# Optimization experiments

Hardware: AMD Instinct MI355X
Metric: run time of the kernel (lower is better)

## Reference

```python
import jax, jax.numpy as jnp
import numpy as np

H_DIM = 256
N_HEADS = 8
HALF = H_DIM // 2

def _lin(x, W, b):
    # torch nn.Linear: y = x @ W.T + b
    y = x @ W.T
    return y + b if b is not None else y

def setup_inputs() -> dict:
    key = jax.random.key(0)
    ks = jax.random.split(key, 16)
    s = 0.02
    d = {
        'x': jax.random.normal(ks[0], (16, H_DIM, 32, 32), jnp.float32),
        'q1_w': jax.random.normal(ks[1], (HALF, HALF), jnp.float32) * s,
        'q1_b': jnp.zeros((HALF,), jnp.float32),
        'q2_w': jax.random.normal(ks[2], (HALF, HALF), jnp.float32) * s,
        'q2_b': jnp.zeros((HALF,), jnp.float32),
        'k1_w': jax.random.normal(ks[3], (HALF, HALF), jnp.float32) * s,
        'k1_b': jnp.zeros((HALF,), jnp.float32),
        'k2_w': jax.random.normal(ks[4], (HALF, HALF), jnp.float32) * s,
        'k2_b': jnp.zeros((HALF,), jnp.float32),
        'v1_w': jax.random.normal(ks[5], (HALF, HALF), jnp.float32) * s,
        'v1_b': jnp.zeros((HALF,), jnp.float32),
        'v2_w': jax.random.normal(ks[6], (HALF, HALF), jnp.float32) * s,
        'v2_b': jnp.zeros((HALF,), jnp.float32),
        'proj1_w': jax.random.normal(ks[7], (HALF, HALF), jnp.float32) * s,
        'proj1_b': jnp.zeros((HALF,), jnp.float32),
        'proj2_w': jax.random.normal(ks[8], (HALF, HALF), jnp.float32) * s,
        'proj2_b': jnp.zeros((HALF,), jnp.float32),
        'logit_scale': jnp.log(10.0 * jnp.ones((N_HEADS, 1, 1), jnp.float32)),
        'mlp_w1': jax.random.normal(ks[9], (128, 2), jnp.float32) * s,
        'mlp_b1': jnp.zeros((128,), jnp.float32),
        'mlp_w2': jax.random.normal(ks[10], (N_HEADS, 128), jnp.float32) * s,
    }
    return d

def _rel_pos_index(h, w):
    # static (numpy) relative position index, shape [N, N]
    ch, cw = np.meshgrid(np.arange(h), np.arange(w), indexing='ij')
    coords = np.stack([ch.reshape(-1), cw.reshape(-1)])  # [2, N]
    rel = coords[:, :, None] - coords[:, None, :]         # [2, N, N]
    rel = rel.transpose(1, 2, 0)
    rel[:, :, 0] += h - 1
    rel[:, :, 1] += w - 1
    return rel[:, :, 0] * (2 * w - 1) + rel[:, :, 1]

def _forward(x, q1_w, q1_b, q2_w, q2_b, k1_w, k1_b, k2_w, k2_b,
             v1_w, v1_b, v2_w, v2_b, proj1_w, proj1_b, proj2_w, proj2_b,
             logit_scale, mlp_w1, mlp_b1, mlp_w2):
    b, c, h, w = x.shape
    N = h * w
    nh = N_HEADS
    hd = c // nh
    x3 = jnp.transpose(x, (0, 2, 3, 1)).reshape(b, N, c)
    x0, x1 = x3[..., :c // 2], x3[..., c // 2:]

    def qkv(W0, b0, W1, b1):
        t = jnp.concatenate([x0 + _lin(x0, W0, b0), x1 + _lin(x1, W1, b1)], axis=-1)
        return t.reshape(b, N, nh, hd).transpose(0, 2, 1, 3)  # [b, nh, N, hd]

    q = qkv(q1_w, q1_b, q2_w, q2_b)
    k = qkv(k1_w, k1_b, k2_w, k2_b)
    v = qkv(v1_w, v1_b, v2_w, v2_b)

    eps = 1e-12
    qn = q / jnp.maximum(jnp.linalg.norm(q, axis=-1, keepdims=True), eps)
    kn = k / jnp.maximum(jnp.linalg.norm(k, axis=-1, keepdims=True), eps)
    attn = jnp.einsum('bhnd,bhmd->bhnm', qn, kn)  # cosine similarity
    scale = jnp.exp(jnp.minimum(logit_scale, jnp.log(1.0 / 0.01)))  # [nh,1,1]
    attn = attn * scale[None]

    # continuous relative-position bias (CPB) table via small MLP
    rch = jnp.arange(-(h - 1), h, dtype=jnp.float32) / (h - 1 + 1e-8)
    rcw = jnp.arange(-(w - 1), w, dtype=jnp.float32) / (w - 1 + 1e-8)
    gh, gw = jnp.meshgrid(rch, rcw, indexing='ij')
    tab = jnp.stack([gh, gw], axis=-1) * 3.2               # [2h-1, 2w-1, 2]
    tab = jnp.sign(tab) * (1.0 - jnp.exp(-jnp.abs(tab)))
    tab = jax.nn.relu(_lin(tab, mlp_w1, mlp_b1))
    tab = _lin(tab, mlp_w2, None).reshape(-1, nh)          # [(2h-1)(2w-1), nh]

    idx = jnp.asarray(_rel_pos_index(h, w))                # [N, N]
    bias = tab[idx.reshape(-1)].reshape(N, N, nh).transpose(2, 0, 1)
    bias = 16.0 * jax.nn.sigmoid(bias)
    attn = attn + bias[None]

    attn = jax.nn.softmax(attn, axis=-1)
    out = jnp.einsum('bhnm,bhmd->bhnd', attn, v).transpose(0, 2, 1, 3).reshape(b, N, c)
    o0, o1 = out[..., :c // 2], out[..., c // 2:]
    out = jnp.concatenate([_lin(o0, proj1_w, proj1_b), _lin(o1, proj2_w, proj2_b)], axis=-1)
    return out.reshape(b, h, w, c).transpose(0, 3, 1, 2)

def reference(x, q1_w, q1_b, q2_w, q2_b, k1_w, k1_b, k2_w, k2_b,
              v1_w, v1_b, v2_w, v2_b, proj1_w, proj1_b, proj2_w, proj2_b,
              logit_scale, mlp_w1, mlp_b1, mlp_w2):
    return _forward(x, q1_w, q1_b, q2_w, q2_b, k1_w, k1_b, k2_w, k2_b,
                    v1_w, v1_b, v2_w, v2_b, proj1_w, proj1_b, proj2_w, proj2_b,
                    logit_scale, mlp_w1, mlp_b1, mlp_w2)
```

## Files before the change

### kernel.cpp

```cpp
#include <hip/hip_runtime.h>
#include <cmath>


typedef _Float16 half_t;
typedef __attribute__((ext_vector_type(4))) _Float16 half4;
typedef __attribute__((ext_vector_type(8))) _Float16 half8;
typedef __attribute__((ext_vector_type(4))) float float4v;

static __device__ __forceinline__ float4v mfma16(half8 a, half8 b, float4v c) {
  return __builtin_amdgcn_mfma_f32_16x16x32_f16(a, b, c, 0, 0, 0);
}

struct PtrArr8 { const float* p[8]; };

__global__ __launch_bounds__(256) void prep_w(PtrArr8 wsrc, PtrArr8 bsrc,
                                              half_t* __restrict__ wf,
                                              float* __restrict__ bws) {
  int y = blockIdx.y;
  const float* src = nullptr;
  const float* bs = nullptr;
#pragma unroll
  for (int i = 0; i < 8; i++)
    if (i == y) { src = wsrc.p[i]; bs = bsrc.p[i]; }
  int i0 = (blockIdx.x * 256 + threadIdx.x) * 4;
  float4 w = *(const float4*)(src + i0);
  int j = i0 >> 7, k = i0 & 127;
  float id0 = 0.f, id1 = 0.f, id2 = 0.f, id3 = 0.f;
  if (y < 6) {
    if (j == k)     id0 = 1.0f;
    if (j == k + 1) id1 = 1.0f;
    if (j == k + 2) id2 = 1.0f;
    if (j == k + 3) id3 = 1.0f;
  }
  half4 h;
  h[0] = (half_t)(w.x + id0);
  h[1] = (half_t)(w.y + id1);
  h[2] = (half_t)(w.z + id2);
  h[3] = (half_t)(w.w + id3);
  *(half4*)(wf + y * 16384 + i0) = h;
  if (blockIdx.x == 0 && threadIdx.x < 128)
    bws[y * 128 + threadIdx.x] = bs[threadIdx.x];
}

__global__ __launch_bounds__(256) void bias_mlp(const float* __restrict__ w1,
                                                const float* __restrict__ b1,
                                                const float* __restrict__ w2,
                                                float* __restrict__ tabh) {
  __shared__ float sw1[256];
  __shared__ float sb1[128];
  __shared__ float sw2[1024];
  int t = threadIdx.x;
  sw1[t] = w1[t];
  if (t < 128) sb1[t] = b1[t];
  for (int i = t; i < 1024; i += 256) sw2[i] = w2[i];
  __syncthreads();
  int p = blockIdx.x * 256 + t;
  if (p >= 3969) return;
  int ph = p / 63, pw = p % 63;
  float t0 = (float)(ph - 31) * (3.2f / 31.0f);
  float t1 = (float)(pw - 31) * (3.2f / 31.0f);
  t0 = copysignf(1.0f - __expf(-fabsf(t0)), t0);
  t1 = copysignf(1.0f - __expf(-fabsf(t1)), t1);
  float acc[8];
#pragma unroll
  for (int hh = 0; hh < 8; hh++) acc[hh] = 0.0f;
  for (int j = 0; j < 128; j++) {
    float hj = fmaxf(0.0f, t0 * sw1[2 * j] + t1 * sw1[2 * j + 1] + sb1[j]);
#pragma unroll
    for (int hh = 0; hh < 8; hh++) acc[hh] += hj * sw2[hh * 128 + j];
  }
#pragma unroll
  for (int hh = 0; hh < 8; hh++)
    tabh[hh * 3969 + p] = 16.0f / (1.0f + __expf(-acc[hh]));
}

__global__ __launch_bounds__(256) void qkv_mfma(
    const float* __restrict__ x, const half_t* __restrict__ wf,
    const float* __restrict__ lscale, const float* __restrict__ bws,
    half_t* __restrict__ qf, half_t* __restrict__ kf,
    half_t* __restrict__ vf) {
  __shared__ half_t yt[128 * 68];
  int t = threadIdx.x;
  int lane = t & 63, wv = t >> 6, l = lane & 15, quad = lane >> 4;
  int m0 = blockIdx.x * 64;
  int b = m0 >> 10, n0 = m0 & 1023;

  half8 afr[8];
  {
    const float* xb = x + (size_t)b * 256 * 1024 + n0 + wv * 16 + l;
#pragma unroll
    for (int hf = 0; hf < 2; hf++)
#pragma unroll
      for (int ks = 0; ks < 4; ks++) {
        int kbase = hf * 128 + ks * 32 + quad * 8;
        half8 a;
#pragma unroll
        for (int j = 0; j < 8; j++)
          a[j] = (half_t)xb[(size_t)(kbase + j) * 1024];
        afr[hf * 4 + ks] = a;
      }
  }

#pragma unroll
  for (int combo = 0; combo < 6; combo++) {
    int op = combo >> 1, hf = combo & 1;
    const half_t* wl = wf + combo * 16384 + l * 128 + quad * 8;
    float4v acc[8];
#pragma unroll
    for (int ng = 0; ng < 8; ng++) {
      float4v c = {0.f, 0.f, 0.f, 0.f};
#pragma unroll
      for (int ks = 0; ks < 4; ks++) {
        half8 bfrag = *(const half8*)(wl + ng * 2048 + ks * 32);
        c = mfma16(afr[hf * 4 + ks], bfrag, c);
      }
      acc[ng] = c;
    }
#pragma unroll
    for (int ng = 0; ng < 8; ng++) {
      float bb = bws[combo * 128 + ng * 16 + l];
#pragma unroll
      for (int r2 = 0; r2 < 4; r2++) acc[ng][r2] += bb;
    }
    if (op < 2) {
#pragma unroll
      for (int hg = 0; hg < 4; hg++) {
        float sc = 1.0f;
        if (op == 0)
          sc = __expf(fminf(lscale[hf * 4 + hg], 4.6051702f));
#pragma unroll
        for (int r2 = 0; r2 < 4; r2++) {
          float ss = acc[2 * hg][r2] * acc[2 * hg][r2] +
                     acc[2 * hg + 1][r2] * acc[2 * hg + 1][r2];
          ss += __shfl_xor(ss, 1, 64);
          ss += __shfl_xor(ss, 2, 64);
          ss += __shfl_xor(ss, 4, 64);
          ss += __shfl_xor(ss, 8, 64);
          float rn = sc / fmaxf(sqrtf(ss), 1e-12f);
          acc[2 * hg][r2] *= rn;
          acc[2 * hg + 1][r2] *= rn;
        }
      }
      half_t* dst = (op == 0) ? qf : kf;
#pragma unroll
      for (int ng = 0; ng < 8; ng++) {
        int head = hf * 4 + (ng >> 1);
        int d = (ng & 1) * 16 + l;
        size_t base =
            (((size_t)b * 8 + head) * 1024 + n0 + wv * 16 + quad * 4) * 32 + d;
#pragma unroll
        for (int r2 = 0; r2 < 4; r2++)
          dst[base + (size_t)r2 * 32] = (half_t)acc[ng][r2];
      }
    } else {
#pragma unroll
      for (int ng = 0; ng < 8; ng++) {
        int col = ng * 16 + l;
        half4 hv;
#pragma unroll
        for (int r2 = 0; r2 < 4; r2++) hv[r2] = (half_t)acc[ng][r2];
        *(half4*)(yt + col * 68 + wv * 16 + quad * 4) = hv;
      }
      __syncthreads();
#pragma unroll
      for (int i = 0; i < 16; i++) {
        int idx = t + 256 * i;
        int col = idx >> 5, rp = idx & 31;
        unsigned int val = *(const unsigned int*)(yt + col * 68 + rp * 2);
        int head = hf * 4 + (col >> 5);
        int d = col & 31;
        *(unsigned int*)((char*)vf +
                         (((((size_t)b * 8 + head) * 32 + d) * 1024) + n0 +
                          rp * 2) * 2) = val;
      }
      __syncthreads();
    }
  }
}

__global__ __launch_bounds__(256) void attn_mfma(
    const half_t* __restrict__ qf, const half_t* __restrict__ kf,
    const half_t* __restrict__ vf, const float* __restrict__ tabh,
    half_t* __restrict__ ao) {
  __shared__ half_t kb[64 * 40];
  __shared__ half_t vt[32 * 72];
  __shared__ half_t pa[4 * 16 * 72];
  __shared__ float sbias[192];

  int t = threadIdx.x;
  int lane = t & 63, wv = t >> 6, l = lane & 15, quad = lane >> 4;
  int qt = blockIdx.x, h = blockIdx.y, b = blockIdx.z;
  int n0 = qt * 64;
  size_t bh = (size_t)b * 8 + h;

  half8 qfr =
      *(const half8*)(qf + (bh * 1024 + n0 + wv * 16 + l) * 32 + quad * 8);

  int qrow_loc = wv * 16 + l;
  int iwq = qrow_loc & 31;
  int ihl = qrow_loc >> 5;

  float run_m = -1e30f, run_l = 0.0f;
  float4v o0 = {0.f, 0.f, 0.f, 0.f}, o1 = {0.f, 0.f, 0.f, 0.f};
  half_t* paw = pa + wv * 16 * 72;

  for (int kt = 0; kt < 16; kt++) {
    __syncthreads();
    {
      int key = t >> 2, dg = t & 3;
      half8 kd =
          *(const half8*)(kf + (bh * 1024 + kt * 64 + key) * 32 + dg * 8);
      *(half8*)(kb + key * 40 + dg * 8) = kd;
      int vd = t >> 3, kg = t & 7;
      half8 vdv =
          *(const half8*)(vf + (bh * 32 + vd) * 1024 + kt * 64 + kg * 8);
      *(half8*)(vt + vd * 72 + kg * 8) = vdv;
      if (t < 189) {
        int r3 = (t >= 126) ? 2 : ((t >= 63) ? 1 : 0);
        int pw = t - r3 * 63;
        int dih = 2 * (qt - kt) + 30 + r3;
        sbias[t] = tabh[h * 3969 + dih * 63 + pw];
      }
    }
    __syncthreads();

    float4v s[4];
#pragma unroll
    for (int nt = 0; nt < 4; nt++) {
      half8 kfr = *(const half8*)(kb + (nt * 16 + l) * 40 + quad * 8);
      float4v z = {0.f, 0.f, 0.f, 0.f};
      s[nt] = mfma16(kfr, qfr, z);
    }
    float lmax = -1e30f;
#pragma unroll
    for (int nt = 0; nt < 4; nt++) {
      int dih_off = ihl - (nt >> 1) + 1;
      int base = dih_off * 63 + iwq + 31 - ((nt & 1) * 16 + 4 * quad);
#pragma unroll
      for (int r2 = 0; r2 < 4; r2++) {
        float v = s[nt][r2] + sbias[base - r2];
        s[nt][r2] = v;
        lmax = fmaxf(lmax, v);
      }
    }
    lmax = fmaxf(lmax, __shfl_xor(lmax, 16, 64));
    lmax = fmaxf(lmax, __shfl_xor(lmax, 32, 64));
    float new_m = fmaxf(run_m, lmax);
    float alpha = __expf(run_m - new_m);
    float lsum = 0.0f;
#pragma unroll
    for (int nt = 0; nt < 4; nt++) {
      half4 ph;
#pragma unroll
      for (int r2 = 0; r2 < 4; r2++) {
        float p = __expf(s[nt][r2] - new_m);
        lsum += p;
        ph[r2] = (half_t)p;
      }
      *(half4*)(paw + l * 72 + nt * 16 + quad * 4) = ph;
    }
    lsum += __shfl_xor(lsum, 16, 64);
    lsum += __shfl_xor(lsum, 32, 64);
    run_l = run_l * alpha + lsum;
    run_m = new_m;
#pragma unroll
    for (int r2 = 0; r2 < 4; r2++) {
      float ar = __shfl(alpha, 20 * quad + r2, 64);
      o0[r2] *= ar;
      o1[r2] *= ar;
    }
#pragma unroll
    for (int ks = 0; ks < 2; ks++) {
      half8 pfr = *(const half8*)(paw + l * 72 + ks * 32 + quad * 8);
      half8 v0f = *(const half8*)(vt + l * 72 + ks * 32 + quad * 8);
      half8 v1f = *(const half8*)(vt + (16 + l) * 72 + ks * 32 + quad * 8);
      o0 = mfma16(pfr, v0f, o0);
      o1 = mfma16(pfr, v1f, o1);
    }
  }

  float rli = 1.0f / run_l;
#pragma unroll
  for (int r2 = 0; r2 < 4; r2++) {
    float linv = __shfl(rli, 20 * quad + r2, 64);
    size_t rowaddr =
        ((size_t)b * 1024 + n0 + wv * 16 + quad * 4 + r2) * 256 + h * 32;
    ao[rowaddr + l] = (half_t)(o0[r2] * linv);
    ao[rowaddr + 16 + l] = (half_t)(o1[r2] * linv);
  }
}

__global__ __launch_bounds__(256) void proj_mfma(
    const half_t* __restrict__ ao, const half_t* __restrict__ wp,
    const float* __restrict__ bws, float* __restrict__ out) {
  __shared__ float yt[128 * 68];
  int t = threadIdx.x;
  int lane = t & 63, wv = t >> 6, l = lane & 15, quad = lane >> 4;
  int m0 = blockIdx.x * 64;
  int b = m0 >> 10, n0 = m0 & 1023;

#pragma unroll
  for (int hf = 0; hf < 2; hf++) {
    half8 afr[4];
    const half_t* ab =
        ao + ((size_t)m0 + wv * 16 + l) * 256 + hf * 128 + quad * 8;
#pragma unroll
    for (int ks = 0; ks < 4; ks++) afr[ks] = *(const half8*)(ab + ks * 32);
    const half_t* wl = wp + hf * 16384 + l * 128 + quad * 8;
#pragma unroll
    for (int ng = 0; ng < 8; ng++) {
      float4v c = {0.f, 0.f, 0.f, 0.f};
#pragma unroll
      for (int ks = 0; ks < 4; ks++)
        c = mfma16(afr[ks], *(const half8*)(wl + ng * 2048 + ks * 32), c);
      float bb = bws[(6 + hf) * 128 + ng * 16 + l];
#pragma unroll
      for (int r2 = 0; r2 < 4; r2++) c[r2] += bb;
      *(float4v*)(yt + (ng * 16 + l) * 68 + wv * 16 + quad * 4) = c;
    }
    __syncthreads();
#pragma unroll
    for (int i = 0; i < 8; i++) {
      int idx = t + 256 * i;
      int col = idx >> 4, rg = idx & 15;
      float4v vv = *(const float4v*)(yt + col * 68 + rg * 4);
      *(float4v*)(out + ((size_t)b * 256 + hf * 128 + col) * 1024 + n0 +
                  rg * 4) = vv;
    }
    __syncthreads();
  }
}

extern "C" void kernel_launch(void* const* d_in, const int* in_sizes, int n_in,
                              void* d_out, int out_size, void* d_ws,
                              size_t ws_size, hipStream_t stream) {
  (void)in_sizes; (void)n_in; (void)out_size; (void)ws_size;
  const float* x = (const float*)d_in[0];

  half_t* ws = (half_t*)d_ws;
  half_t* qfp = ws;
  half_t* kfp = ws + 4194304;
  half_t* vfp = ws + 8388608;
  half_t* aop = ws + 12582912;
  half_t* wfp = ws + 16777216;
  float* tabh = (float*)((char*)d_ws + 33816576);
  float* bws = (float*)((char*)d_ws + 33943584);

  PtrArr8 wsrc, bsrc;
  const int widx[8] = {1, 3, 5, 7, 9, 11, 13, 15};
  for (int i = 0; i < 8; i++) {
    wsrc.p[i] = (const float*)d_in[widx[i]];
    bsrc.p[i] = (const float*)d_in[widx[i] + 1];
  }

  prep_w<<<dim3(16, 8), 256, 0, stream>>>(wsrc, bsrc, wfp, bws);
  bias_mlp<<<16, 256, 0, stream>>>((const float*)d_in[18],
                                   (const float*)d_in[19],
                                   (const float*)d_in[20], tabh);
  qkv_mfma<<<256, 256, 0, stream>>>(x, wfp, (const float*)d_in[17], bws, qfp,
                                    kfp, vfp);
  attn_mfma<<<dim3(16, 8, 16), 256, 0, stream>>>(qfp, kfp, vfp, tabh, aop);
  proj_mfma<<<256, 256, 0, stream>>>(aop, wfp + 6 * 16384, bws,
                                     (float*)d_out);
}
```

Baseline: 228.7 us.

## Split qkv/proj grids by half, prefetch K/V, and drop online softmax max

The qkv and proj kernels now launch a second grid dimension over the two channel halves, which doubles the block count and shrinks per-block register use. The attention kernel prefetches the next K/V tile and bias slice into registers while computing the current tile. Because the cosine logits and the sigmoid bias are bounded, it replaces the online-softmax running max and rescaling with a fixed upper-bound offset. The bias is also fed directly as the MFMA accumulator input, and exp2 is used in place of exp. This relies on bounded logits for numerical safety and removes one barrier per iteration.

Measured after the change: 209.2 us. 8.6% less time.

```diff
diff --git a/kernel.cpp b/kernel.cpp
--- a/kernel.cpp
+++ b/kernel.cpp
@@ -82,28 +82,27 @@
   __shared__ half_t yt[128 * 68];
   int t = threadIdx.x;
   int lane = t & 63, wv = t >> 6, l = lane & 15, quad = lane >> 4;
+  int hf = blockIdx.y;
   int m0 = blockIdx.x * 64;
   int b = m0 >> 10, n0 = m0 & 1023;
 
-  half8 afr[8];
+  half8 afr[4];
   {
     const float* xb = x + (size_t)b * 256 * 1024 + n0 + wv * 16 + l;
 #pragma unroll
-    for (int hf = 0; hf < 2; hf++)
-#pragma unroll
-      for (int ks = 0; ks < 4; ks++) {
-        int kbase = hf * 128 + ks * 32 + quad * 8;
-        half8 a;
-#pragma unroll
-        for (int j = 0; j < 8; j++)
-          a[j] = (half_t)xb[(size_t)(kbase + j) * 1024];
-        afr[hf * 4 + ks] = a;
-      }
-  }
-
-#pragma unroll
-  for (int combo = 0; combo < 6; combo++) {
-    int op = combo >> 1, hf = combo & 1;
+    for (int ks = 0; ks < 4; ks++) {
+      int kbase = hf * 128 + ks * 32 + quad * 8;
+      half8 a;
+#pragma unroll
+      for (int j = 0; j < 8; j++)
+        a[j] = (half_t)xb[(size_t)(kbase + j) * 1024];
+      afr[ks] = a;
+    }
+  }
+
+#pragma unroll
+  for (int op = 0; op < 3; op++) {
+    int combo = op * 2 + hf;
     const half_t* wl = wf + combo * 16384 + l * 128 + quad * 8;
     float4v acc[8];
 #pragma unroll
@@ -112,7 +111,7 @@
 #pragma unroll
       for (int ks = 0; ks < 4; ks++) {
         half8 bfrag = *(const half8*)(wl + ng * 2048 + ks * 32);
-        c = mfma16(afr[hf * 4 + ks], bfrag, c);
+        c = mfma16(afr[ks], bfrag, c);
       }
       acc[ng] = c;
     }
@@ -173,7 +172,6 @@
                          (((((size_t)b * 8 + head) * 32 + d) * 1024) + n0 +
                           rp * 2) * 2) = val;
       }
-      __syncthreads();
     }
   }
 }
@@ -181,7 +179,7 @@
 __global__ __launch_bounds__(256) void attn_mfma(
     const half_t* __restrict__ qf, const half_t* __restrict__ kf,
     const half_t* __restrict__ vf, const float* __restrict__ tabh,
-    half_t* __restrict__ ao) {
+    const float* __restrict__ lscale, half_t* __restrict__ ao) {
   __shared__ half_t kb[64 * 40];
   __shared__ half_t vt[32 * 72];
   __shared__ half_t pa[4 * 16 * 72];
@@ -192,6 +190,8 @@
   int qt = blockIdx.x, h = blockIdx.y, b = blockIdx.z;
   int n0 = qt * 64;
   size_t bh = (size_t)b * 8 + h;
+  float scale = __expf(fminf(lscale[h], 4.6051702f));
+  float c14 = 14.0f - (scale + 16.0f) * 1.44269504f;
 
   half8 qfr =
       *(const half8*)(qf + (bh * 1024 + n0 + wv * 16 + l) * 32 + quad * 8);
@@ -200,74 +200,58 @@
   int iwq = qrow_loc & 31;
   int ihl = qrow_loc >> 5;
 
-  float run_m = -1e30f, run_l = 0.0f;
+  float run_l = 0.0f;
   float4v o0 = {0.f, 0.f, 0.f, 0.f}, o1 = {0.f, 0.f, 0.f, 0.f};
   half_t* paw = pa + wv * 16 * 72;
 
+  int key_s = t >> 2, dg_s = t & 3;
+  int vd_s = t >> 3, kg_s = t & 7;
+  int r3 = (t >= 126) ? 2 : ((t >= 63) ? 1 : 0);
+  int pw_s = t - r3 * 63;
+
+  half8 kreg = *(const half8*)(kf + (bh * 1024 + key_s) * 32 + dg_s * 8);
+  half8 vreg = *(const half8*)(vf + (bh * 32 + vd_s) * 1024 + kg_s * 8);
+  float breg = 0.0f;
+  if (t < 189) breg = tabh[h * 3969 + (2 * qt + 30 + r3) * 63 + pw_s];
+
   for (int kt = 0; kt < 16; kt++) {
+    *(half8*)(kb + key_s * 40 + dg_s * 8) = kreg;
+    *(half8*)(vt + vd_s * 72 + kg_s * 8) = vreg;
+    if (t < 189) sbias[t] = breg;
     __syncthreads();
-    {
-      int key = t >> 2, dg = t & 3;
-      half8 kd =
-          *(const half8*)(kf + (bh * 1024 + kt * 64 + key) * 32 + dg * 8);
-      *(half8*)(kb + key * 40 + dg * 8) = kd;
-      int vd = t >> 3, kg = t & 7;
-      half8 vdv =
-          *(const half8*)(vf + (bh * 32 + vd) * 1024 + kt * 64 + kg * 8);
-      *(half8*)(vt + vd * 72 + kg * 8) = vdv;
-      if (t < 189) {
-        int r3 = (t >= 126) ? 2 : ((t >= 63) ? 1 : 0);
-        int pw = t - r3 * 63;
-        int dih = 2 * (qt - kt) + 30 + r3;
-        sbias[t] = tabh[h * 3969 + dih * 63 + pw];
-      }
-    }
-    __syncthreads();
+    if (kt < 15) {
+      kreg = *(const half8*)(kf +
+                             (bh * 1024 + (kt + 1) * 64 + key_s) * 32 +
+                             dg_s * 8);
+      vreg = *(const half8*)(vf + (bh * 32 + vd_s) * 1024 + (kt + 1) * 64 +
+                             kg_s * 8);
+      if (t < 189)
+        breg = tabh[h * 3969 + (2 * (qt - kt - 1) + 30 + r3) * 63 + pw_s];
+    }
 
     float4v s[4];
 #pragma unroll
     for (int nt = 0; nt < 4; nt++) {
+      int base = (ihl - (nt >> 1) + 1) * 63 + iwq + 31 -
+                 ((nt & 1) * 16 + 4 * quad);
+      float4v c;
+      c[0] = sbias[base];
+      c[1] = sbias[base - 1];
+      c[2] = sbias[base - 2];
+      c[3] = sbias[base - 3];
       half8 kfr = *(const half8*)(kb + (nt * 16 + l) * 40 + quad * 8);
-      float4v z = {0.f, 0.f, 0.f, 0.f};
-      s[nt] = mfma16(kfr, qfr, z);
-    }
-    float lmax = -1e30f;
-#pragma unroll
-    for (int nt = 0; nt < 4; nt++) {
-      int dih_off = ihl - (nt >> 1) + 1;
-      int base = dih_off * 63 + iwq + 31 - ((nt & 1) * 16 + 4 * quad);
-#pragma unroll
-      for (int r2 = 0; r2 < 4; r2++) {
-        float v = s[nt][r2] + sbias[base - r2];
-        s[nt][r2] = v;
-        lmax = fmaxf(lmax, v);
-      }
-    }
-    lmax = fmaxf(lmax, __shfl_xor(lmax, 16, 64));
-    lmax = fmaxf(lmax, __shfl_xor(lmax, 32, 64));
-    float new_m = fmaxf(run_m, lmax);
-    float alpha = __expf(run_m - new_m);
-    float lsum = 0.0f;
+      s[nt] = mfma16(kfr, qfr, c);
+    }
 #pragma unroll
     for (int nt = 0; nt < 4; nt++) {
       half4 ph;
 #pragma unroll
       for (int r2 = 0; r2 < 4; r2++) {
-        float p = __expf(s[nt][r2] - new_m);
-        lsum += p;
+        float p = exp2f(fmaf(s[nt][r2], 1.44269504f, c14));
+        run_l += p;
         ph[r2] = (half_t)p;
       }
       *(half4*)(paw + l * 72 + nt * 16 + quad * 4) = ph;
-    }
-    lsum += __shfl_xor(lsum, 16, 64);
-    lsum += __shfl_xor(lsum, 32, 64);
-    run_l = run_l * alpha + lsum;
-    run_m = new_m;
-#pragma unroll
-    for (int r2 = 0; r2 < 4; r2++) {
-      float ar = __shfl(alpha, 20 * quad + r2, 64);
-      o0[r2] *= ar;
-      o1[r2] *= ar;
     }
 #pragma unroll
     for (int ks = 0; ks < 2; ks++) {
@@ -277,9 +261,13 @@
       o0 = mfma16(pfr, v0f, o0);
       o1 = mfma16(pfr, v1f, o1);
     }
-  }
-
+    __syncthreads();
+  }
+
+  run_l += __shfl_xor(run_l, 16, 64);
+  run_l += __shfl_xor(run_l, 32, 64);
   float rli = 1.0f / run_l;
+
 #pragma unroll
   for (int r2 = 0; r2 < 4; r2++) {
     float linv = __shfl(rli, 20 * quad + r2, 64);
@@ -296,38 +284,35 @@
   __shared__ float yt[128 * 68];
   int t = threadIdx.x;
   int lane = t & 63, wv = t >> 6, l = lane & 15, quad = lane >> 4;
+  int hf = blockIdx.y;
   int m0 = blockIdx.x * 64;
   int b = m0 >> 10, n0 = m0 & 1023;
 
-#pragma unroll
-  for (int hf = 0; hf < 2; hf++) {
-    half8 afr[4];
-    const half_t* ab =
-        ao + ((size_t)m0 + wv * 16 + l) * 256 + hf * 128 + quad * 8;
-#pragma unroll
-    for (int ks = 0; ks < 4; ks++) afr[ks] = *(const half8*)(ab + ks * 32);
-    const half_t* wl = wp + hf * 16384 + l * 128 + quad * 8;
-#pragma unroll
-    for (int ng = 0; ng < 8; ng++) {
-      float4v c = {0.f, 0.f, 0.f, 0.f};
-#pragma unroll
-      for (int ks = 0; ks < 4; ks++)
-        c = mfma16(afr[ks], *(const half8*)(wl + ng * 2048 + ks * 32), c);
-      float bb = bws[(6 + hf) * 128 + ng * 16 + l];
-#pragma unroll
-      for (int r2 = 0; r2 < 4; r2++) c[r2] += bb;
-      *(float4v*)(yt + (ng * 16 + l) * 68 + wv * 16 + quad * 4) = c;
-    }
-    __syncthreads();
-#pragma unroll
-    for (int i = 0; i < 8; i++) {
-      int idx = t + 256 * i;
-      int col = idx >> 4, rg = idx & 15;
-      float4v vv = *(const float4v*)(yt + col * 68 + rg * 4);
-      *(float4v*)(out + ((size_t)b * 256 + hf * 128 + col) * 1024 + n0 +
-                  rg * 4) = vv;
-    }
-    __syncthreads();
+  half8 afr[4];
+  const half_t* ab =
+      ao + ((size_t)m0 + wv * 16 + l) * 256 + hf * 128 + quad * 8;
+#pragma unroll
+  for (int ks = 0; ks < 4; ks++) afr[ks] = *(const half8*)(ab + ks * 32);
+  const half_t* wl = wp + hf * 16384 + l * 128 + quad * 8;
+#pragma unroll
+  for (int ng = 0; ng < 8; ng++) {
+    float4v c = {0.f, 0.f, 0.f, 0.f};
+#pragma unroll
+    for (int ks = 0; ks < 4; ks++)
+      c = mfma16(afr[ks], *(const half8*)(wl + ng * 2048 + ks * 32), c);
+    float bb = bws[(6 + hf) * 128 + ng * 16 + l];
+#pragma unroll
+    for (int r2 = 0; r2 < 4; r2++) c[r2] += bb;
+    *(float4v*)(yt + (ng * 16 + l) * 68 + wv * 16 + quad * 4) = c;
+  }
+  __syncthreads();
+#pragma unroll
+  for (int i = 0; i < 8; i++) {
+    int idx = t + 256 * i;
+    int col = idx >> 4, rg = idx & 15;
+    float4v vv = *(const float4v*)(yt + col * 68 + rg * 4);
+    *(float4v*)(out + ((size_t)b * 256 + hf * 128 + col) * 1024 + n0 +
+                rg * 4) = vv;
   }
 }
 
@@ -357,9 +342,10 @@
   bias_mlp<<<16, 256, 0, stream>>>((const float*)d_in[18],
                                    (const float*)d_in[19],
                                    (const float*)d_in[20], tabh);
-  qkv_mfma<<<256, 256, 0, stream>>>(x, wfp, (const float*)d_in[17], bws, qfp,
-                                    kfp, vfp);
-  attn_mfma<<<dim3(16, 8, 16), 256, 0, stream>>>(qfp, kfp, vfp, tabh, aop);
-  proj_mfma<<<256, 256, 0, stream>>>(aop, wfp + 6 * 16384, bws,
-                                     (float*)d_out);
-}
+  qkv_mfma<<<dim3(256, 2), 256, 0, stream>>>(x, wfp, (const float*)d_in[17],
+                                             bws, qfp, kfp, vfp);
+  attn_mfma<<<dim3(16, 8, 16), 256, 0, stream>>>(
+      qfp, kfp, vfp, tabh, (const float*)d_in[17], aop);
+  proj_mfma<<<dim3(256, 2), 256, 0, stream>>>(aop, wfp + 6 * 16384, bws,
+                                              (float*)d_out);
+}
```
